# Kernel tuning notes

Hardware: AMD Instinct MI355X
Metric: run time of the kernel (lower is better)

The kernel has to match this reference:

```python
import jax, jax.numpy as jnp
import numpy as np

B, S, C = 64, 4096, 128
TARGET_LEN = 1000  # Resizing1D(length=1000)


def setup_inputs() -> dict:
    key = jax.random.key(0)
    k1, k2 = jax.random.split(key)
    inputs = jax.random.normal(k1, (B, S, C), dtype=jnp.float32)
    # Sequence mask: True for the first `len` positions of each row (what
    # masked_lengths inverts). Lengths in [S//2, S] -> genuine ragged resize.
    lengths = jax.random.randint(k2, (B,), S // 2, S + 1)
    mask = jnp.arange(S)[None, :] < lengths[:, None]
    return {"inputs": inputs, "mask": mask}


def masked_lengths(mask):
    # inverse of tf.sequence_mask: S - index of first True in the reversed row
    s = mask.shape[1]
    return (s - jnp.argmax(mask[:, ::-1], axis=1)).astype(jnp.int32)  # [B]


def reference(inputs, mask):
    """Per-sample variable-length bilinear resize to TARGET_LEN.

    Matches tf.image.resize(method='bilinear', half_pixel_centers=True)
    applied to inputs[b, :lengths[b], :] for each sample b, fully batched.
    """
    lengths = masked_lengths(mask)                                  # [B]
    scale = lengths.astype(jnp.float32) / TARGET_LEN                # [B]
    # half-pixel-center source coordinates, per sample: [B, L]
    src = (jnp.arange(TARGET_LEN, dtype=jnp.float32)[None, :] + 0.5) * scale[:, None] - 0.5
    maxi = (lengths - 1)[:, None]                                   # [B, 1]
    lo = jnp.clip(jnp.floor(src).astype(jnp.int32), 0, maxi)        # [B, L]
    hi = jnp.clip(jnp.ceil(src).astype(jnp.int32), 0, maxi)         # [B, L]
    w = src - lo.astype(jnp.float32)                                # lerp weight
    # Gather along the sequence axis: [B, L, C]
    xlo = jnp.take_along_axis(inputs, lo[:, :, None], axis=1)
    xhi = jnp.take_along_axis(inputs, hi[:, :, None], axis=1)
    # When lo == hi (clamped edge) the w term cancels, matching TF kernel.
    return xlo + (xhi - xlo) * w[:, :, None]
```

## Files before the change

### kernel.cpp

```cpp
#include <hip/hip_runtime.h>
#include <hip/hip_bf16.h>
#include <stdint.h>

#define B_DIM 64
#define S_DIM 4096
#define C_DIM 128
#define TARGET_LEN 1000

__global__ void lengths_kernel(const void* __restrict__ mask_raw,
                               int* __restrict__ lengths) {
    const int b = blockIdx.x;
    const int tid = threadIdx.x;

    const uint32_t first = *(const uint32_t*)mask_raw;

    int cnt = 0;
    if (first == 0x01010101u) {
        const uint8_t* m = (const uint8_t*)mask_raw + (size_t)b * S_DIM;
        for (int i = tid; i < S_DIM; i += blockDim.x) cnt += (m[i] != 0);
    } else if (first == 0x3F800000u) {
        const float* m = (const float*)mask_raw + (size_t)b * S_DIM;
        for (int i = tid; i < S_DIM; i += blockDim.x) cnt += (m[i] != 0.0f);
    } else {
        const int* m = (const int*)mask_raw + (size_t)b * S_DIM;
        for (int i = tid; i < S_DIM; i += blockDim.x) cnt += (m[i] != 0);
    }

    for (int off = 32; off > 0; off >>= 1) cnt += __shfl_down(cnt, off);

    __shared__ int sdata[4];
    const int wave = tid >> 6;
    const int lane = tid & 63;
    if (lane == 0) sdata[wave] = cnt;
    __syncthreads();
    if (tid == 0) {
        lengths[b] = sdata[0] + sdata[1] + sdata[2] + sdata[3];
    }
}

__global__ void resize_kernel(const float* __restrict__ in,
                              const int* __restrict__ lengths,
                              float* __restrict__ out) {
    const int C4 = C_DIM / 4;
    int idx = blockIdx.x * blockDim.x + threadIdx.x;
    const int total = B_DIM * TARGET_LEN * C4;
    if (idx >= total) return;

    const int c4 = idx & (C4 - 1);
    const int bl = idx >> 5;
    const int l  = bl % TARGET_LEN;
    const int b  = bl / TARGET_LEN;

    const int len = lengths[b];
    const float scale = __fdiv_rn((float)len, (float)TARGET_LEN);
    const float t   = __fadd_rn((float)l, 0.5f);
    const float src = __fsub_rn(__fmul_rn(t, scale), 0.5f);

    const int maxi = len - 1;
    int lo = (int)floorf(src);
    int hi = (int)ceilf(src);
    lo = min(max(lo, 0), maxi);
    hi = min(max(hi, 0), maxi);
    const float w = __fsub_rn(src, (float)lo);

    const size_t base = (size_t)b * S_DIM * C_DIM;
    const float4 xlo = *(const float4*)(in + base + (size_t)lo * C_DIM + c4 * 4);
    const float4 xhi = *(const float4*)(in + base + (size_t)hi * C_DIM + c4 * 4);

    float4 r;
    r.x = __fadd_rn(xlo.x, __fmul_rn(__fsub_rn(xhi.x, xlo.x), w));
    r.y = __fadd_rn(xlo.y, __fmul_rn(__fsub_rn(xhi.y, xlo.y), w));
    r.z = __fadd_rn(xlo.z, __fmul_rn(__fsub_rn(xhi.z, xlo.z), w));
    r.w = __fadd_rn(xlo.w, __fmul_rn(__fsub_rn(xhi.w, xlo.w), w));

    *(float4*)(out + (size_t)bl * C_DIM + c4 * 4) = r;
}

extern "C" void kernel_launch(void* const* d_in, const int* in_sizes, int n_in,
                              void* d_out, int out_size, void* d_ws, size_t ws_size,
                              hipStream_t stream) {
    const float* in   = (const float*)d_in[0];
    const void*  mask = d_in[1];
    float* out = (float*)d_out;
    int* lengths = (int*)d_ws;

    lengths_kernel<<<B_DIM, 256, 0, stream>>>(mask, lengths);

    const int total = B_DIM * TARGET_LEN * (C_DIM / 4);
    resize_kernel<<<(total + 255) / 256, 256, 0, stream>>>(in, lengths, out);
}
```

Baseline: 195.5 us.

## Fuse mask length reduction into resize kernel with vectorized popcount

```diff
diff --git a/kernel.cpp b/kernel.cpp
--- a/kernel.cpp
+++ b/kernel.cpp
@@ -6,55 +6,58 @@
 #define S_DIM 4096
 #define C_DIM 128
 #define TARGET_LEN 1000
+#define ROWS_PER_BLOCK 8
 
-__global__ void lengths_kernel(const void* __restrict__ mask_raw,
-                               int* __restrict__ lengths) {
-    const int b = blockIdx.x;
-    const int tid = threadIdx.x;
+__global__ __launch_bounds__(256) void fused_resize_kernel(
+    const float* __restrict__ in,
+    const void* __restrict__ mask_raw,
+    float* __restrict__ out) {
+    const int b     = blockIdx.y;
+    const int chunk = blockIdx.x;
+    const int tid   = threadIdx.x;
 
     const uint32_t first = *(const uint32_t*)mask_raw;
 
     int cnt = 0;
     if (first == 0x01010101u) {
-        const uint8_t* m = (const uint8_t*)mask_raw + (size_t)b * S_DIM;
-        for (int i = tid; i < S_DIM; i += blockDim.x) cnt += (m[i] != 0);
+        const uint4* m = (const uint4*)((const uint8_t*)mask_raw + (size_t)b * S_DIM);
+        uint4 v = m[tid];
+        cnt = __popc(v.x) + __popc(v.y) + __popc(v.z) + __popc(v.w);
     } else if (first == 0x3F800000u) {
-        const float* m = (const float*)mask_raw + (size_t)b * S_DIM;
-        for (int i = tid; i < S_DIM; i += blockDim.x) cnt += (m[i] != 0.0f);
+        const float4* m = (const float4*)((const float*)mask_raw + (size_t)b * S_DIM);
+        #pragma unroll
+        for (int k = 0; k < 4; ++k) {
+            float4 v = m[tid + k * 256];
+            cnt += (v.x != 0.0f) + (v.y != 0.0f) + (v.z != 0.0f) + (v.w != 0.0f);
+        }
     } else {
-        const int* m = (const int*)mask_raw + (size_t)b * S_DIM;
-        for (int i = tid; i < S_DIM; i += blockDim.x) cnt += (m[i] != 0);
+        const uint4* m = (const uint4*)((const int*)mask_raw + (size_t)b * S_DIM);
+        #pragma unroll
+        for (int k = 0; k < 4; ++k) {
+            uint4 v = m[tid + k * 256];
+            cnt += __popc(v.x) + __popc(v.y) + __popc(v.z) + __popc(v.w);
+        }
     }
 
+    #pragma unroll
     for (int off = 32; off > 0; off >>= 1) cnt += __shfl_down(cnt, off);
 
     __shared__ int sdata[4];
+    __shared__ int s_len;
     const int wave = tid >> 6;
     const int lane = tid & 63;
     if (lane == 0) sdata[wave] = cnt;
     __syncthreads();
-    if (tid == 0) {
-        lengths[b] = sdata[0] + sdata[1] + sdata[2] + sdata[3];
-    }
-}
+    if (tid == 0) s_len = sdata[0] + sdata[1] + sdata[2] + sdata[3];
+    __syncthreads();
+    const int len = s_len;
 
-__global__ void resize_kernel(const float* __restrict__ in,
-                              const int* __restrict__ lengths,
-                              float* __restrict__ out) {
-    const int C4 = C_DIM / 4;
-    int idx = blockIdx.x * blockDim.x + threadIdx.x;
-    const int total = B_DIM * TARGET_LEN * C4;
-    if (idx >= total) return;
+    const int c4 = tid & 31;
+    const int l  = chunk * ROWS_PER_BLOCK + (tid >> 5);
 
-    const int c4 = idx & (C4 - 1);
-    const int bl = idx >> 5;
-    const int l  = bl % TARGET_LEN;
-    const int b  = bl / TARGET_LEN;
-
-    const int len = lengths[b];
     const float scale = __fdiv_rn((float)len, (float)TARGET_LEN);
-    const float t   = __fadd_rn((float)l, 0.5f);
-    const float src = __fsub_rn(__fmul_rn(t, scale), 0.5f);
+    const float t     = __fadd_rn((float)l, 0.5f);
+    const float src   = __fsub_rn(__fmul_rn(t, scale), 0.5f);
 
     const int maxi = len - 1;
     int lo = (int)floorf(src);
@@ -73,7 +76,8 @@
     r.z = __fadd_rn(xlo.z, __fmul_rn(__fsub_rn(xhi.z, xlo.z), w));
     r.w = __fadd_rn(xlo.w, __fmul_rn(__fsub_rn(xhi.w, xlo.w), w));
 
-    *(float4*)(out + (size_t)bl * C_DIM + c4 * 4) = r;
+    const size_t obase = ((size_t)b * TARGET_LEN + l) * C_DIM + c4 * 4;
+    *(float4*)(out + obase) = r;
 }
 
 extern "C" void kernel_launch(void* const* d_in, const int* in_sizes, int n_in,
@@ -82,10 +86,7 @@
     const float* in   = (const float*)d_in[0];
     const void*  mask = d_in[1];
     float* out = (float*)d_out;
-    int* lengths = (int*)d_ws;
 
-    lengths_kernel<<<B_DIM, 256, 0, stream>>>(mask, lengths);
-
-    const int total = B_DIM * TARGET_LEN * (C_DIM / 4);
-    resize_kernel<<<(total + 255) / 256, 256, 0, stream>>>(in, lengths, out);
+    dim3 grid(TARGET_LEN / ROWS_PER_BLOCK, B_DIM);
+    fused_resize_kernel<<<grid, 256, 0, stream>>>(in, mask, out);
 }
```

Measured after the change: 191.0 us. 1.02x faster.
